# Performance work log

Hardware: AMD Instinct MI355X
Metric: run time of the kernel (lower is better)

Reference implementation:

```python
import jax, jax.numpy as jnp
import numpy as np

B, D, T = 16, 512, 2048
H = 2
HD = D // H

def setup_inputs() -> dict:
    key = jax.random.key(0)
    k1, k2, k3, k4 = jax.random.split(key, 4)
    s_in = 1.0 / np.sqrt(D)   # torch default-like uniform init for weight_matrix
    s_t = 1.0 / np.sqrt(T)    # nn.Linear default init bound
    xs = jax.random.normal(k1, (B, D, T), dtype=jnp.float32)
    W_KQ = jax.random.uniform(k2, (D, D), jnp.float32, -s_in, s_in)
    W_PV = jax.random.uniform(k3, (D, D), jnp.float32, -s_in, s_in)
    W_out = jax.random.uniform(k4, (T, T), jnp.float32, -s_t, s_t)
    return {"xs": xs, "W_KQ": W_KQ, "W_PV": W_PV, "W_out": W_out}

def reference(xs, W_KQ, W_PV, W_out):
    b, d, t = xs.shape
    xs_skip = xs[:, :, :-1]                                   # [B, D, T-1]
    # xskq = xs_skip^T @ W_KQ  -> [B, T-1, D]
    xskq = jnp.einsum('bds,dj->bsj', xs_skip, W_KQ)
    # split heads: [B, H, T-1, HD]
    xskq_split = xskq.reshape(b, t - 1, H, HD).transpose(0, 2, 1, 3)
    # xs reshaped to heads along feature dim: [B, H, HD, T]
    xs_r = xs.reshape(b, H, HD, t)
    attn_arg = jnp.matmul(xskq_split, xs_r)                   # [B, H, T-1, T], rho=1
    # NON-STANDARD: softmax over the head axis (size 2)
    sm = jax.nn.softmax(attn_arg, axis=1)
    # W_PV @ xs_skip -> [B, D, T-1], split into heads [B, H, HD, T-1]
    wpvx = jnp.einsum('id,bds->bis', W_PV, xs_skip).reshape(b, H, HD, t - 1)
    f_attn = jnp.matmul(wpvx, sm).reshape(b, d, t)            # [B, D, T]
    # output = Linear(T, T, bias=None) then take last token:
    # out[b, i] = sum_t f_attn[b, i, t] * W_out[T-1, t]
    out = jnp.einsum('bdt,t->bd', f_attn, W_out[-1])
    return out
```

## Files before the change

kernel.cpp:

```cpp
#include <hip/hip_runtime.h>
#include <hip/hip_bf16.h>

#define NB 16
#define ND 512
#define NT 2048
#define TM1 2047
#define NHD 256

typedef __attribute__((ext_vector_type(8))) short bf16x8;
typedef __attribute__((ext_vector_type(4))) float f32x4;
typedef unsigned short ushort_t;
typedef unsigned int uint_t;

#define G0_OFF    0ull
#define G0_ELEMS  (16ull * 2047ull)
#define WSUM_OFF  32752ull
#define R_OFF     32768ull
#define WKQT_OFF  49152ull
#define CHUNK_OFF 180224ull
#define BATCH_US  (2048ull * 512ull)
#define BATCH_FLOATS (2ull * 524288ull)

__device__ __forceinline__ ushort_t f2bf(float x) {
    union { float f; uint_t u; } v; v.f = x;
    uint_t r = v.u + 0x7FFFu + ((v.u >> 16) & 1u);
    return (ushort_t)(r >> 16);
}

__device__ __forceinline__ void async_copy16(const ushort_t* g, ushort_t* l) {
    __builtin_amdgcn_global_load_lds(
        (const __attribute__((address_space(1))) void*)g,
        (__attribute__((address_space(3))) void*)l, 16, 0, 0);
}

__global__ __launch_bounds__(256) void k_prep(const float* __restrict__ wkq,
                                              ushort_t* __restrict__ wkqT,
                                              const float* __restrict__ wlast,
                                              float* __restrict__ wsum,
                                              float* __restrict__ g0) {
    __shared__ float tile[32][33];
    const int j0 = blockIdx.x * 32, d0 = blockIdx.y * 32;
    const int c = threadIdx.x & 31, r = threadIdx.x >> 5;
    #pragma unroll
    for (int i = 0; i < 4; ++i) {
        const int d = r + i * 8;
        tile[d][c] = wkq[(size_t)(d0 + d) * ND + j0 + c];
    }
    __syncthreads();
    #pragma unroll
    for (int i = 0; i < 4; ++i) {
        const int j = r + i * 8;
        wkqT[(size_t)(j0 + j) * ND + d0 + c] = f2bf(tile[c][j]);
    }
    const int bid = blockIdx.y * 16 + blockIdx.x;
    if (threadIdx.x < 128) {
        const int idx = bid * 128 + threadIdx.x;
        if (idx < (int)G0_ELEMS) g0[idx] = 0.f;
    }
    if (bid == 0) {
        __shared__ float red[256];
        float s = 0.f;
        for (int t = threadIdx.x; t < NT; t += 256) s += wlast[t];
        red[threadIdx.x] = s;
        __syncthreads();
        for (int off = 128; off > 0; off >>= 1) {
            if (threadIdx.x < off) red[threadIdx.x] += red[threadIdx.x + off];
            __syncthreads();
        }
        if (threadIdx.x == 0) *wsum = red[0];
    }
}

__global__ __launch_bounds__(256) void k_cvt_xst(const float* __restrict__ xs,
                                                 ushort_t* __restrict__ xst, int b0) {
    __shared__ float tile[32][33];
    const int t0 = blockIdx.x * 32, d0 = blockIdx.y * 32;
    const int cc = blockIdx.z;
    const int b = b0 + cc;
    const int c = threadIdx.x & 31, r = threadIdx.x >> 5;
    const float* xb = xs + (size_t)b * ND * NT;
    ushort_t* xo = xst + (size_t)cc * BATCH_US;
    #pragma unroll
    for (int i = 0; i < 4; ++i) {
        const int d = r + i * 8;
        tile[d][c] = xb[(size_t)(d0 + d) * NT + t0 + c];
    }
    __syncthreads();
    #pragma unroll
    for (int i = 0; i < 4; ++i) {
        const int t = r + i * 8;
        xo[(size_t)(t0 + t) * ND + d0 + c] = f2bf(tile[c][t]);
    }
}

__global__ __launch_bounds__(256) void k_qd(const ushort_t* __restrict__ xst,
                                            const ushort_t* __restrict__ wkqT,
                                            ushort_t* __restrict__ qdb) {
    const int j0 = blockIdx.x * 128;
    const int s0 = blockIdx.y * 128;
    const int cc = blockIdx.z;
    __shared__ __align__(16) ushort_t As[128 * 64];
    __shared__ __align__(16) ushort_t Bs[128 * 64];
    const int tid = threadIdx.x;
    const int wave = tid >> 6, lane = tid & 63;
    const int l15 = lane & 15, quad = lane >> 4;
    const int wm = wave >> 1, wn = wave & 1;
    const int swz = l15 & 7;
    const int lrow = lane >> 3;
    const size_t lsrc = (size_t)lrow * ND + (size_t)(((lane & 7) ^ lrow) << 3);
    const ushort_t* xa = xst + (size_t)cc * BATCH_US + (size_t)s0 * ND;
    const ushort_t* wb = wkqT + (size_t)j0 * ND;
    ushort_t* qo = qdb + (size_t)cc * BATCH_US;
    f32x4 acc[4][4];
    #pragma unroll
    for (int mi = 0; mi < 4; ++mi)
        #pragma unroll
        for (int nj = 0; nj < 4; ++nj) acc[mi][nj] = (f32x4){0.f, 0.f, 0.f, 0.f};
    for (int ks = 0; ks < 8; ++ks) {
        const int k0 = ks * 64;
        #pragma unroll
        for (int n = 0; n < 4; ++n) {
            const int rbase = wave * 32 + n * 8;
            async_copy16(xa + (size_t)rbase * ND + k0 + lsrc, &As[rbase * 64]);
            async_copy16(wb + (size_t)rbase * ND + k0 + lsrc, &Bs[rbase * 64]);
        }
        __builtin_amdgcn_s_waitcnt(0);
        __syncthreads();
        #pragma unroll
        for (int kc = 0; kc < 2; ++kc) {
            bf16x8 af[4], bfr[4];
            #pragma unroll
            for (int mi = 0; mi < 4; ++mi)
                af[mi] = *(const bf16x8*)&As[(wm * 64 + mi * 16 + l15) * 64 + (((kc * 4 + quad) ^ swz) << 3)];
            #pragma unroll
            for (int nj = 0; nj < 4; ++nj)
                bfr[nj] = *(const bf16x8*)&Bs[(wn * 64 + nj * 16 + l15) * 64 + (((kc * 4 + quad) ^ swz) << 3)];
            #pragma unroll
            for (int mi = 0; mi < 4; ++mi)
                #pragma unroll
                for (int nj = 0; nj < 4; ++nj)
                    acc[mi][nj] = __builtin_amdgcn_mfma_f32_16x16x32_bf16(af[mi], bfr[nj], acc[mi][nj], 0, 0, 0);
        }
        __syncthreads();
    }
    #pragma unroll
    for (int mi = 0; mi < 4; ++mi) {
        const int srow = s0 + wm * 64 + mi * 16 + quad * 4;
        #pragma unroll
        for (int nj = 0; nj < 4; ++nj) {
            const int jcol = j0 + wn * 64 + nj * 16 + l15;
            const float sgn = (jcol < NHD) ? 1.f : -1.f;
            #pragma unroll
            for (int r = 0; r < 4; ++r)
                qo[(size_t)(srow + r) * ND + jcol] = f2bf(sgn * acc[mi][nj][r]);
        }
    }
}

__global__ __launch_bounds__(256) void k_attn(const ushort_t* __restrict__ qdb,
                                              const ushort_t* __restrict__ xst,
                                              const float* __restrict__ wlast,
                                              float* __restrict__ g0, int b0) {
    const int t0 = blockIdx.x * 128;
    const int s0 = blockIdx.y * 128;
    const int cc = blockIdx.z;
    const int b = b0 + cc;
    __shared__ __align__(16) ushort_t As[128 * 64];
    __shared__ __align__(16) ushort_t Bs[128 * 64];
    const int tid = threadIdx.x;
    const int wave = tid >> 6, lane = tid & 63;
    const int l15 = lane & 15, quad = lane >> 4;
    const int wm = wave >> 1, wn = wave & 1;
    const int swz = l15 & 7;
    const int lrow = lane >> 3;
    const size_t lsrc = (size_t)lrow * ND + (size_t)(((lane & 7) ^ lrow) << 3);
    const ushort_t* qa = qdb + (size_t)cc * BATCH_US + (size_t)s0 * ND;
    const ushort_t* xa = xst + (size_t)cc * BATCH_US + (size_t)t0 * ND;
    f32x4 acc[4][4];
    #pragma unroll
    for (int mi = 0; mi < 4; ++mi)
        #pragma unroll
        for (int nj = 0; nj < 4; ++nj) acc[mi][nj] = (f32x4){0.f, 0.f, 0.f, 0.f};
    for (int ks = 0; ks < 8; ++ks) {
        const int k0 = ks * 64;
        #pragma unroll
        for (int n = 0; n < 4; ++n) {
            const int rbase = wave * 32 + n * 8;
            async_copy16(qa + (size_t)rbase * ND + k0 + lsrc, &As[rbase * 64]);
            async_copy16(xa + (size_t)rbase * ND + k0 + lsrc, &Bs[rbase * 64]);
        }
        __builtin_amdgcn_s_waitcnt(0);
        __syncthreads();
        #pragma unroll
        for (int kc = 0; kc < 2; ++kc) {
            bf16x8 af[4], bfr[4];
            #pragma unroll
            for (int mi = 0; mi < 4; ++mi)
                af[mi] = *(const bf16x8*)&As[(wm * 64 + mi * 16 + l15) * 64 + (((kc * 4 + quad) ^ swz) << 3)];
            #pragma unroll
            for (int nj = 0; nj < 4; ++nj)
                bfr[nj] = *(const bf16x8*)&Bs[(wn * 64 + nj * 16 + l15) * 64 + (((kc * 4 + quad) ^ swz) << 3)];
            #pragma unroll
            for (int mi = 0; mi < 4; ++mi)
                #pragma unroll
                for (int nj = 0; nj < 4; ++nj)
                    acc[mi][nj] = __builtin_amdgcn_mfma_f32_16x16x32_bf16(af[mi], bfr[nj], acc[mi][nj], 0, 0, 0);
        }
        __syncthreads();
    }
    float gp[4][4] = {};
    #pragma unroll
    for (int nj = 0; nj < 4; ++nj) {
        const float wt = wlast[t0 + wn * 64 + nj * 16 + l15];
        #pragma unroll
        for (int mi = 0; mi < 4; ++mi)
            #pragma unroll
            for (int r = 0; r < 4; ++r) {
                const float e = __expf(-acc[mi][nj][r]);
                const float sg = __builtin_amdgcn_rcpf(1.f + e);
                gp[mi][r] = fmaf(sg, wt, gp[mi][r]);
            }
    }
    #pragma unroll
    for (int mi = 0; mi < 4; ++mi)
        #pragma unroll
        for (int r = 0; r < 4; ++r) {
            float v = gp[mi][r];
            v += __shfl_xor(v, 1);
            v += __shfl_xor(v, 2);
            v += __shfl_xor(v, 4);
            v += __shfl_xor(v, 8);
            if (l15 == 0) {
                const int srow = s0 + wm * 64 + mi * 16 + quad * 4 + r;
                if (srow < TM1) atomicAdd(&g0[b * TM1 + srow], v);
            }
        }
}

__global__ __launch_bounds__(256) void k_r(const float* __restrict__ xs,
                                           const float* __restrict__ g0,
                                           const float* __restrict__ wsum,
                                           float* __restrict__ r) {
    const int d = blockIdx.x;
    const int b = blockIdx.y;
    const float* xrow = xs + ((size_t)b * ND + d) * NT;
    const float* g = g0 + b * TM1;
    float a0 = 0.f, a1 = 0.f;
    for (int s = threadIdx.x; s < TM1; s += 256) {
        const float x = xrow[s];
        a0 = fmaf(x, g[s], a0);
        a1 += x;
    }
    #pragma unroll
    for (int off = 32; off > 0; off >>= 1) {
        a0 += __shfl_down(a0, off);
        a1 += __shfl_down(a1, off);
    }
    __shared__ float l0[4], l1[4];
    const int wid = threadIdx.x >> 6;
    if ((threadIdx.x & 63) == 0) { l0[wid] = a0; l1[wid] = a1; }
    __syncthreads();
    if (threadIdx.x == 0) {
        const float sum0 = l0[0] + l0[1] + l0[2] + l0[3];
        const float sumx = l1[0] + l1[1] + l1[2] + l1[3];
        const float wsv = *wsum;
        r[((size_t)b * 2 + 0) * ND + d] = sum0;
        r[((size_t)b * 2 + 1) * ND + d] = fmaf(wsv, sumx, -sum0);
    }
}

__global__ __launch_bounds__(256) void k_out(const float* __restrict__ wpv,
                                             const float* __restrict__ r,
                                             float* __restrict__ out) {
    const int b = blockIdx.x;
    __shared__ float rs[1024];
    for (int i = threadIdx.x; i < 1024; i += 256) rs[i] = r[(size_t)b * 1024 + i];
    __syncthreads();
    for (int i = threadIdx.x; i < ND; i += 256) {
        const float* wrow = wpv + (size_t)i * ND;
        const float* rh = rs + (i >> 8) * ND;
        float acc = 0.f;
        for (int dd = 0; dd < ND; dd += 4) {
            const float4 wv = *(const float4*)(wrow + dd);
            acc += wv.x * rh[dd] + wv.y * rh[dd + 1] + wv.z * rh[dd + 2] + wv.w * rh[dd + 3];
        }
        out[b * ND + i] = acc;
    }
}

extern "C" void kernel_launch(void* const* d_in, const int* in_sizes, int n_in,
                              void* d_out, int out_size, void* d_ws, size_t ws_size,
                              hipStream_t stream) {
    (void)in_sizes; (void)n_in; (void)out_size;
    const float* xs   = (const float*)d_in[0];
    const float* wkq  = (const float*)d_in[1];
    const float* wpv  = (const float*)d_in[2];
    const float* wout = (const float*)d_in[3];
    const float* wlast = wout + (size_t)(NT - 1) * NT;

    float* ws   = (float*)d_ws;
    float* g0   = ws + G0_OFF;
    float* wsum = ws + WSUM_OFF;
    float* r    = ws + R_OFF;
    ushort_t* wkqT = (ushort_t*)(ws + WKQT_OFF);

    const size_t ws_floats = ws_size / 4;
    size_t avail = (ws_floats > CHUNK_OFF) ? (ws_floats - CHUNK_OFF) : 0;
    int C = (int)(avail / BATCH_FLOATS);
    if (C > NB) C = NB;
    if (C < 1) C = 1;
    ushort_t* qdb = (ushort_t*)(ws + CHUNK_OFF);
    ushort_t* xst = (ushort_t*)(ws + CHUNK_OFF + (size_t)C * 524288ull);

    k_prep<<<dim3(16, 16), 256, 0, stream>>>(wkq, wkqT, wlast, wsum, g0);
    for (int b0 = 0; b0 < NB; b0 += C) {
        const int cb = (NB - b0 < C) ? (NB - b0) : C;
        k_cvt_xst<<<dim3(64, 16, cb), 256, 0, stream>>>(xs, xst, b0);
        k_qd     <<<dim3(4, 16, cb),  256, 0, stream>>>(xst, wkqT, qdb);
        k_attn   <<<dim3(16, 16, cb), 256, 0, stream>>>(qdb, xst, wlast, g0, b0);
    }
    k_r  <<<dim3(ND, NB), 256, 0, stream>>>(xs, g0, wsum, r);
    k_out<<<NB, 256, 0, stream>>>(wpv, r, (float*)d_out);
}
```

Baseline: 310.8 us.

## Compute reductions from bf16 transposed xs per chunk and widen transpose tiles

The r reduction now reads the bf16 transposed copy of xs already produced per chunk, instead of re-reading the full fp32 xs after all chunks. It accumulates partial sums with atomics, and the final combination with wsum moves into k_out. The transpose kernel uses 64x64 tiles with float4 loads and packed bf16 stores. This cuts a large fp32 re-read, but the reduction now uses bf16-rounded inputs and adds atomics over a larger zeroed workspace.

```diff
diff --git a/kernel.cpp b/kernel.cpp
--- a/kernel.cpp
+++ b/kernel.cpp
@@ -14,10 +14,12 @@
 
 #define G0_OFF    0ull
 #define G0_ELEMS  (16ull * 2047ull)
-#define WSUM_OFF  32752ull
-#define R_OFF     32768ull
-#define WKQT_OFF  49152ull
-#define CHUNK_OFF 180224ull
+#define R0_OFF    32768ull
+#define SX_OFF    40960ull
+#define ZERO_FLOATS 49152ull
+#define WSUM_OFF  49152ull
+#define WKQT_OFF  49408ull
+#define CHUNK_OFF 180480ull
 #define BATCH_US  (2048ull * 512ull)
 #define BATCH_FLOATS (2ull * 524288ull)
 
@@ -26,6 +28,10 @@
     uint_t r = v.u + 0x7FFFu + ((v.u >> 16) & 1u);
     return (ushort_t)(r >> 16);
 }
+__device__ __forceinline__ float bf2f(uint_t u) {
+    union { uint_t u; float f; } v; v.u = u << 16;
+    return v.f;
+}
 
 __device__ __forceinline__ void async_copy16(const ushort_t* g, ushort_t* l) {
     __builtin_amdgcn_global_load_lds(
@@ -37,7 +43,7 @@
                                               ushort_t* __restrict__ wkqT,
                                               const float* __restrict__ wlast,
                                               float* __restrict__ wsum,
-                                              float* __restrict__ g0) {
+                                              float* __restrict__ zbase) {
     __shared__ float tile[32][33];
     const int j0 = blockIdx.x * 32, d0 = blockIdx.y * 32;
     const int c = threadIdx.x & 31, r = threadIdx.x >> 5;
@@ -53,10 +59,7 @@
         wkqT[(size_t)(j0 + j) * ND + d0 + c] = f2bf(tile[c][j]);
     }
     const int bid = blockIdx.y * 16 + blockIdx.x;
-    if (threadIdx.x < 128) {
-        const int idx = bid * 128 + threadIdx.x;
-        if (idx < (int)G0_ELEMS) g0[idx] = 0.f;
-    }
+    if (threadIdx.x < 192) zbase[bid * 192 + threadIdx.x] = 0.f;
     if (bid == 0) {
         __shared__ float red[256];
         float s = 0.f;
@@ -73,23 +76,26 @@
 
 __global__ __launch_bounds__(256) void k_cvt_xst(const float* __restrict__ xs,
                                                  ushort_t* __restrict__ xst, int b0) {
-    __shared__ float tile[32][33];
-    const int t0 = blockIdx.x * 32, d0 = blockIdx.y * 32;
+    __shared__ float tile[64][65];
+    const int t0 = blockIdx.x * 64, d0 = blockIdx.y * 64;
     const int cc = blockIdx.z;
-    const int b = b0 + cc;
-    const int c = threadIdx.x & 31, r = threadIdx.x >> 5;
-    const float* xb = xs + (size_t)b * ND * NT;
+    const float* xb = xs + (size_t)(b0 + cc) * ND * NT;
     ushort_t* xo = xst + (size_t)cc * BATCH_US;
+    const int r = threadIdx.x >> 4;
+    const int c4 = (threadIdx.x & 15) * 4;
     #pragma unroll
     for (int i = 0; i < 4; ++i) {
-        const int d = r + i * 8;
-        tile[d][c] = xb[(size_t)(d0 + d) * NT + t0 + c];
+        const int d = r + i * 16;
+        *(float4*)&tile[d][c4] = *(const float4*)&xb[(size_t)(d0 + d) * NT + t0 + c4];
     }
     __syncthreads();
     #pragma unroll
     for (int i = 0; i < 4; ++i) {
-        const int t = r + i * 8;
-        xo[(size_t)(t0 + t) * ND + d0 + c] = f2bf(tile[c][t]);
+        const int t = r + i * 16;
+        const uint_t p0 = (uint_t)f2bf(tile[c4 + 0][t]) | ((uint_t)f2bf(tile[c4 + 1][t]) << 16);
+        const uint_t p1 = (uint_t)f2bf(tile[c4 + 2][t]) | ((uint_t)f2bf(tile[c4 + 3][t]) << 16);
+        uint2 pk; pk.x = p0; pk.y = p1;
+        *(uint2*)&xo[(size_t)(t0 + t) * ND + d0 + c4] = pk;
     }
 }
 
@@ -237,44 +243,47 @@
         }
 }
 
-__global__ __launch_bounds__(256) void k_r(const float* __restrict__ xs,
+__global__ __launch_bounds__(256) void k_r(const ushort_t* __restrict__ xst,
                                            const float* __restrict__ g0,
-                                           const float* __restrict__ wsum,
-                                           float* __restrict__ r) {
-    const int d = blockIdx.x;
-    const int b = blockIdx.y;
-    const float* xrow = xs + ((size_t)b * ND + d) * NT;
+                                           float* __restrict__ r0acc,
+                                           float* __restrict__ sxacc, int b0) {
+    const int sc = blockIdx.x;
+    const int cc = blockIdx.y;
+    const int b = b0 + cc;
+    const ushort_t* xa = xst + (size_t)cc * BATCH_US;
     const float* g = g0 + b * TM1;
-    float a0 = 0.f, a1 = 0.f;
-    for (int s = threadIdx.x; s < TM1; s += 256) {
-        const float x = xrow[s];
-        a0 = fmaf(x, g[s], a0);
-        a1 += x;
-    }
-    #pragma unroll
-    for (int off = 32; off > 0; off >>= 1) {
-        a0 += __shfl_down(a0, off);
-        a1 += __shfl_down(a1, off);
-    }
-    __shared__ float l0[4], l1[4];
-    const int wid = threadIdx.x >> 6;
-    if ((threadIdx.x & 63) == 0) { l0[wid] = a0; l1[wid] = a1; }
-    __syncthreads();
-    if (threadIdx.x == 0) {
-        const float sum0 = l0[0] + l0[1] + l0[2] + l0[3];
-        const float sumx = l1[0] + l1[1] + l1[2] + l1[3];
-        const float wsv = *wsum;
-        r[((size_t)b * 2 + 0) * ND + d] = sum0;
-        r[((size_t)b * 2 + 1) * ND + d] = fmaf(wsv, sumx, -sum0);
-    }
+    const int d2 = threadIdx.x;
+    float a00 = 0.f, a01 = 0.f, a10 = 0.f, a11 = 0.f;
+    const int send = (sc == 7) ? 255 : 256;
+    for (int si = 0; si < send; ++si) {
+        const int s = sc * 256 + si;
+        const float gv = g[s];
+        const uint_t pk = *(const uint_t*)&xa[(size_t)s * ND + d2 * 2];
+        const float x0 = bf2f(pk & 0xFFFFu);
+        const float x1 = bf2f(pk >> 16);
+        a00 = fmaf(x0, gv, a00); a01 = fmaf(x1, gv, a01);
+        a10 += x0; a11 += x1;
+    }
+    atomicAdd(&r0acc[b * ND + d2 * 2], a00);
+    atomicAdd(&r0acc[b * ND + d2 * 2 + 1], a01);
+    atomicAdd(&sxacc[b * ND + d2 * 2], a10);
+    atomicAdd(&sxacc[b * ND + d2 * 2 + 1], a11);
 }
 
 __global__ __launch_bounds__(256) void k_out(const float* __restrict__ wpv,
-                                             const float* __restrict__ r,
+                                             const float* __restrict__ r0acc,
+                                             const float* __restrict__ sxacc,
+                                             const float* __restrict__ wsum,
                                              float* __restrict__ out) {
     const int b = blockIdx.x;
     __shared__ float rs[1024];
-    for (int i = threadIdx.x; i < 1024; i += 256) rs[i] = r[(size_t)b * 1024 + i];
+    const float wsv = *wsum;
+    for (int i = threadIdx.x; i < ND; i += 256) {
+        const float r0 = r0acc[b * ND + i];
+        const float sx = sxacc[b * ND + i];
+        rs[i] = r0;
+        rs[ND + i] = fmaf(wsv, sx, -r0);
+    }
     __syncthreads();
     for (int i = threadIdx.x; i < ND; i += 256) {
         const float* wrow = wpv + (size_t)i * ND;
@@ -298,10 +307,11 @@
     const float* wout = (const float*)d_in[3];
     const float* wlast = wout + (size_t)(NT - 1) * NT;
 
-    float* ws   = (float*)d_ws;
-    float* g0   = ws + G0_OFF;
-    float* wsum = ws + WSUM_OFF;
-    float* r    = ws + R_OFF;
+    float* ws    = (float*)d_ws;
+    float* g0    = ws + G0_OFF;
+    float* r0acc = ws + R0_OFF;
+    float* sxacc = ws + SX_OFF;
+    float* wsum  = ws + WSUM_OFF;
     ushort_t* wkqT = (ushort_t*)(ws + WKQT_OFF);
 
     const size_t ws_floats = ws_size / 4;
@@ -312,13 +322,13 @@
     ushort_t* qdb = (ushort_t*)(ws + CHUNK_OFF);
     ushort_t* xst = (ushort_t*)(ws + CHUNK_OFF + (size_t)C * 524288ull);
 
-    k_prep<<<dim3(16, 16), 256, 0, stream>>>(wkq, wkqT, wlast, wsum, g0);
+    k_prep<<<dim3(16, 16), 256, 0, stream>>>(wkq, wkqT, wlast, wsum, ws);
     for (int b0 = 0; b0 < NB; b0 += C) {
         const int cb = (NB - b0 < C) ? (NB - b0) : C;
-        k_cvt_xst<<<dim3(64, 16, cb), 256, 0, stream>>>(xs, xst, b0);
+        k_cvt_xst<<<dim3(32, 8, cb), 256, 0, stream>>>(xs, xst, b0);
         k_qd     <<<dim3(4, 16, cb),  256, 0, stream>>>(xst, wkqT, qdb);
         k_attn   <<<dim3(16, 16, cb), 256, 0, stream>>>(qdb, xst, wlast, g0, b0);
-    }
-    k_r  <<<dim3(ND, NB), 256, 0, stream>>>(xs, g0, wsum, r);
-    k_out<<<NB, 256, 0, stream>>>(wpv, r, (float*)d_out);
-}
+        k_r      <<<dim3(8, cb),      256, 0, stream>>>(xst, g0, r0acc, sxacc, b0);
+    }
+    k_out<<<NB, 256, 0, stream>>>(wpv, r0acc, sxacc, wsum, (float*)d_out);
+}
```

Result: slower. 344.1 us (+10.7%).
